# Kernel optimization log

Hardware: AMD Instinct MI355X
Metric: run time of the kernel (lower is better)

The kernel has to match this reference:

```python
import jax, jax.numpy as jnp
import numpy as np

N_LIG, N_TGT, E = 100000, 20000, 250000
LIG_IN, TGT_IN, H = 4, 1280, 128


def setup_inputs() -> dict:
    key = jax.random.key(0)
    ks = jax.random.split(key, 12)
    def lin_w(k, fan_in, fan_out):
        # kaiming-uniform-ish init, stored as [in, out] for x @ W
        bound = 1.0 / np.sqrt(fan_in)
        return jax.random.uniform(k, (fan_in, fan_out), jnp.float32, -bound, bound)
    return {
        "x_ligand": jax.random.normal(ks[0], (N_LIG, LIG_IN), jnp.float32),
        "x_target": jax.random.normal(ks[1], (N_TGT, TGT_IN), jnp.float32),
        "edge_src": jax.random.randint(ks[2], (E,), 0, N_LIG, jnp.int32),
        "edge_dst": jax.random.randint(ks[3], (E,), 0, N_TGT, jnp.int32),
        # SAGEConv (ligand -> target): lin_l on aggregated ligand msgs, lin_r on target self
        "W_lt_l": lin_w(ks[4], LIG_IN, H),
        "b_lt_l": jnp.zeros((H,), jnp.float32),
        "W_lt_r": lin_w(ks[5], TGT_IN, H),
        # SAGEConv (target -> ligand): lin_l on aggregated target msgs, lin_r on ligand self
        "W_tl_l": lin_w(ks[6], TGT_IN, H),
        "b_tl_l": jnp.zeros((H,), jnp.float32),
        "W_tl_r": lin_w(ks[7], LIG_IN, H),
        # edge predictor: Linear(2H -> 1)
        "W_ep": lin_w(ks[8], 2 * H, 1),
        "b_ep": jnp.zeros((1,), jnp.float32),
    }


def _mean_agg(x_src, src_idx, dst_idx, num_dst):
    # gather per-edge source features, scatter-mean onto destination nodes
    msg = x_src[src_idx]                                             # [E, F]
    s = jax.ops.segment_sum(msg, dst_idx, num_segments=num_dst)      # [N_dst, F]
    cnt = jax.ops.segment_sum(jnp.ones((src_idx.shape[0], 1), x_src.dtype),
                              dst_idx, num_segments=num_dst)         # [N_dst, 1]
    return s / jnp.maximum(cnt, 1.0)


def reference(x_ligand, x_target, edge_src, edge_dst,
              W_lt_l, b_lt_l, W_lt_r, W_tl_l, b_tl_l, W_tl_r, W_ep, b_ep):
    # SAGEConv (ligand, binds_to, target): aggregate ligand msgs into targets
    agg_t = _mean_agg(x_ligand, edge_src, edge_dst, N_TGT)           # [N_TGT, LIG_IN]
    t_out = agg_t @ W_lt_l + b_lt_l + x_target @ W_lt_r              # [N_TGT, H]
    # SAGEConv (target, binds_to, ligand): reversed edges (flip(0))
    agg_l = _mean_agg(x_target, edge_dst, edge_src, N_LIG)           # [N_LIG, TGT_IN]
    l_out = agg_l @ W_tl_l + b_tl_l + x_ligand @ W_tl_r              # [N_LIG, H]
    l_out = jax.nn.relu(l_out)
    t_out = jax.nn.relu(t_out)
    # edge predictor: gather endpoints, concat, linear, squeeze
    edge_feats = jnp.concatenate([l_out[edge_src], t_out[edge_dst]], axis=-1)  # [E, 2H]
    out = (edge_feats @ W_ep + b_ep).squeeze(-1)                     # [E]
    return out
```

## Files before the change

### kernel.cpp

```cpp
#include <hip/hip_runtime.h>
#include <hip/hip_bf16.h>


#define H 128
#define K_DIM 1280
#define LIG_IN 4
#define CAP_L 24
#define CAP_T 48

typedef __attribute__((ext_vector_type(8))) short bf16x8;
typedef __attribute__((ext_vector_type(4))) float f32x4;

#define AS1(p) ((const __attribute__((address_space(1))) void*)(p))
#define AS3(p) ((__attribute__((address_space(3))) void*)(p))

__global__ void fill_both(const int* __restrict__ src, const int* __restrict__ dst,
                          int* __restrict__ cur_l, int* __restrict__ cur_t,
                          int* __restrict__ adjd, int* __restrict__ adjs, int E)
{
    int e = blockIdx.x * blockDim.x + threadIdx.x;
    if (e >= E) return;
    int s = src[e], d = dst[e];
    int p = atomicAdd(&cur_l[s], 1);
    adjd[s * CAP_L + p] = d;
    int q = atomicAdd(&cur_t[d], 1);
    adjs[d * CAP_T + q] = s;
}

__global__ void cast_wt(const float* __restrict__ Wl, const float* __restrict__ Wr,
                        __hip_bfloat16* __restrict__ Wt, int n)
{
    int idx = blockIdx.x * blockDim.x + threadIdx.x;
    if (idx >= n) return;
    int nr = idx / K_DIM, k = idx - nr * K_DIM;
    float v = (nr < H) ? Wl[k * H + nr] : Wr[k * H + (nr - H)];
    Wt[idx] = __float2bfloat16(v);
}

__global__ __launch_bounds__(256)
void gemm_fused(const float* __restrict__ Xf,
                const unsigned short* __restrict__ Wt,
                float* __restrict__ y_tl, float* __restrict__ t_lin, int M)
{
    __shared__ short As[64 * 32];
    __shared__ short Bs[256 * 32];

    const int bm = blockIdx.x * 64;
    const int w = threadIdx.x >> 6, lane = threadIdx.x & 63;
    const int mrow = lane & 15, quad = lane >> 4;

    const int a_row = threadIdx.x >> 2;
    const int a_seg = threadIdx.x & 3;
    const float* gA = Xf + (size_t)min(bm + a_row, M - 1) * K_DIM + a_seg * 8;
    char* lA = (char*)As + a_row * 64 + a_seg * 16;

    const unsigned short* gB[4];
    char* lB[4];
#pragma unroll
    for (int i = 0; i < 4; ++i) {
        int q = i * 64 + lane;
        int row = w * 64 + (q >> 2);
        int seg = q & 3;
        gB[i] = Wt + (size_t)row * K_DIM + seg * 8;
        lB[i] = (char*)Bs + w * 4096 + i * 1024 + lane * 16;
    }

    f32x4 acc[4][4];
#pragma unroll
    for (int i = 0; i < 4; ++i)
#pragma unroll
        for (int j = 0; j < 4; ++j)
            acc[i][j] = (f32x4){0.f, 0.f, 0.f, 0.f};

    for (int k0 = 0; k0 < K_DIM; k0 += 32) {
#pragma unroll
        for (int i = 0; i < 4; ++i)
            __builtin_amdgcn_global_load_lds(AS1(gB[i] + k0), AS3(lB[i]), 16, 0, 0);
        float4 v0 = *(const float4*)(gA + k0);
        float4 v1 = *(const float4*)(gA + k0 + 4);
        union { __hip_bfloat16 h[8]; uint4 u; } r;
        r.h[0] = __float2bfloat16(v0.x); r.h[1] = __float2bfloat16(v0.y);
        r.h[2] = __float2bfloat16(v0.z); r.h[3] = __float2bfloat16(v0.w);
        r.h[4] = __float2bfloat16(v1.x); r.h[5] = __float2bfloat16(v1.y);
        r.h[6] = __float2bfloat16(v1.z); r.h[7] = __float2bfloat16(v1.w);
        *(uint4*)lA = r.u;
        __syncthreads();

        bf16x8 aF[4], bF[4];
#pragma unroll
        for (int i = 0; i < 4; ++i)
            aF[i] = *(const bf16x8*)((const char*)As + (i * 16 + mrow) * 64 + quad * 16);
#pragma unroll
        for (int j = 0; j < 4; ++j)
            bF[j] = *(const bf16x8*)((const char*)Bs + (w * 64 + j * 16 + mrow) * 64 + quad * 16);
#pragma unroll
        for (int i = 0; i < 4; ++i)
#pragma unroll
            for (int j = 0; j < 4; ++j)
                acc[i][j] = __builtin_amdgcn_mfma_f32_16x16x32_bf16(aF[i], bF[j], acc[i][j], 0, 0, 0);
        __syncthreads();
    }

    float* __restrict__ Y = (w < 2) ? y_tl : t_lin;
    const int cbase = (w & 1) * 64;
#pragma unroll
    for (int i = 0; i < 4; ++i) {
#pragma unroll
        for (int r = 0; r < 4; ++r) {
            int row = bm + i * 16 + quad * 4 + r;
            if (row < M) {
#pragma unroll
                for (int j = 0; j < 4; ++j) {
                    int col = cbase + j * 16 + mrow;
                    Y[(size_t)row * H + col] = acc[i][j][r];
                }
            }
        }
    }
}

__global__ void target_post(const int* __restrict__ cur_t, const int* __restrict__ adjs,
                            const float* __restrict__ xl, const float* __restrict__ t_lin,
                            const float* __restrict__ W_lt_l, const float* __restrict__ b_lt_l,
                            const float* __restrict__ W_ep,
                            float* __restrict__ st, int NT)
{
    int wid = (blockIdx.x * blockDim.x + threadIdx.x) >> 6;
    int lane = threadIdx.x & 63;
    if (wid >= NT) return;
    int cnt = cur_t[wid];
    float a0 = 0.f, a1 = 0.f, a2 = 0.f, a3 = 0.f;
    for (int j = lane; j < cnt; j += 64) {
        int s = adjs[wid * CAP_T + j];
        float4 v = *(const float4*)(xl + (size_t)s * LIG_IN);
        a0 += v.x; a1 += v.y; a2 += v.z; a3 += v.w;
    }
#pragma unroll
    for (int off = 32; off > 0; off >>= 1) {
        a0 += __shfl_xor(a0, off);
        a1 += __shfl_xor(a1, off);
        a2 += __shfl_xor(a2, off);
        a3 += __shfl_xor(a3, off);
    }
    float inv = 1.0f / fmaxf((float)cnt, 1.0f);
    a0 *= inv; a1 *= inv; a2 *= inv; a3 *= inv;
    float acc = 0.f;
#pragma unroll
    for (int p = 0; p < 2; ++p) {
        int h = lane + p * 64;
        float v = a0 * W_lt_l[h] + a1 * W_lt_l[H + h] + a2 * W_lt_l[2 * H + h] +
                  a3 * W_lt_l[3 * H + h] + b_lt_l[h] + t_lin[(size_t)wid * H + h];
        v = fmaxf(v, 0.f);
        acc += v * W_ep[H + h];
    }
#pragma unroll
    for (int off = 32; off > 0; off >>= 1) acc += __shfl_down(acc, off);
    if (lane == 0) st[wid] = acc;
}

__global__ void ligand_gather_post(const int* __restrict__ cur_l, const int* __restrict__ adjd,
                                   const float* __restrict__ y_tl,
                                   const float* __restrict__ xl,
                                   const float* __restrict__ W_tl_r, const float* __restrict__ b_tl_l,
                                   const float* __restrict__ W_ep,
                                   float* __restrict__ sl, int NL)
{
    int wid = (blockIdx.x * blockDim.x + threadIdx.x) >> 6;
    int lane = threadIdx.x & 63;
    if (wid >= NL) return;
    int cnt = cur_l[wid];
    float a0 = 0.f, a1 = 0.f;
    for (int j = 0; j < cnt; ++j) {
        int d = adjd[wid * CAP_L + j];
        const float* row = y_tl + (size_t)d * H;
        a0 += row[lane];
        a1 += row[lane + 64];
    }
    float inv = 1.0f / fmaxf((float)cnt, 1.0f);
    float4 x = *(const float4*)(xl + (size_t)wid * LIG_IN);
    float acc = 0.f;
    {
        int h = lane;
        float v = a0 * inv + b_tl_l[h] +
                  x.x * W_tl_r[h] + x.y * W_tl_r[H + h] +
                  x.z * W_tl_r[2 * H + h] + x.w * W_tl_r[3 * H + h];
        v = fmaxf(v, 0.f);
        acc += v * W_ep[h];
    }
    {
        int h = lane + 64;
        float v = a1 * inv + b_tl_l[h] +
                  x.x * W_tl_r[h] + x.y * W_tl_r[H + h] +
                  x.z * W_tl_r[2 * H + h] + x.w * W_tl_r[3 * H + h];
        v = fmaxf(v, 0.f);
        acc += v * W_ep[h];
    }
#pragma unroll
    for (int off = 32; off > 0; off >>= 1) acc += __shfl_down(acc, off);
    if (lane == 0) sl[wid] = acc;
}

__global__ void edge_out(const int* __restrict__ src, const int* __restrict__ dst,
                         const float* __restrict__ sl, const float* __restrict__ st,
                         const float* __restrict__ b_ep, float* __restrict__ out, int E)
{
    int e = blockIdx.x * blockDim.x + threadIdx.x;
    if (e >= E) return;
    out[e] = sl[src[e]] + st[dst[e]] + b_ep[0];
}

extern "C" void kernel_launch(void* const* d_in, const int* in_sizes, int n_in,
                              void* d_out, int out_size, void* d_ws, size_t ws_size,
                              hipStream_t stream) {
    const float* x_ligand = (const float*)d_in[0];
    const float* x_target = (const float*)d_in[1];
    const int*   edge_src = (const int*)d_in[2];
    const int*   edge_dst = (const int*)d_in[3];
    const float* W_lt_l   = (const float*)d_in[4];
    const float* b_lt_l   = (const float*)d_in[5];
    const float* W_lt_r   = (const float*)d_in[6];
    const float* W_tl_l   = (const float*)d_in[7];
    const float* b_tl_l   = (const float*)d_in[8];
    const float* W_tl_r   = (const float*)d_in[9];
    const float* W_ep     = (const float*)d_in[10];
    const float* b_ep     = (const float*)d_in[11];
    float* out = (float*)d_out;

    const int NL = in_sizes[0] / LIG_IN;
    const int NT = in_sizes[1] / K_DIM;
    const int E  = in_sizes[2];

    char* ws = (char*)d_ws;
    size_t off = 0;
    auto take = [&](size_t bytes) { size_t o = off; off += (bytes + 15) & ~(size_t)15; return o; };
    size_t off_Wt     = take((size_t)2 * H * K_DIM * 2);
    size_t off_y_tl   = take((size_t)NT * H * 4);
    size_t off_t_lin  = take((size_t)NT * H * 4);
    size_t off_adjd   = take((size_t)NL * CAP_L * 4);
    size_t off_adjs   = take((size_t)NT * CAP_T * 4);
    size_t off_cur_l  = take((size_t)NL * 4);
    size_t off_cur_t  = take((size_t)NT * 4);
    size_t off_sl     = take((size_t)NL * 4);
    size_t off_st     = take((size_t)NT * 4);
    if (off > ws_size) {
        hipMemsetAsync(d_out, 0, (size_t)out_size * 4, stream);
        return;
    }

    __hip_bfloat16* Wt = (__hip_bfloat16*)(ws + off_Wt);
    float* y_tl  = (float*)(ws + off_y_tl);
    float* t_lin = (float*)(ws + off_t_lin);
    int*   adjd  = (int*)(ws + off_adjd);
    int*   adjs  = (int*)(ws + off_adjs);
    int*   cur_l = (int*)(ws + off_cur_l);
    int*   cur_t = (int*)(ws + off_cur_t);
    float* sl    = (float*)(ws + off_sl);
    float* st    = (float*)(ws + off_st);

    hipMemsetAsync(cur_l, 0, off_sl - off_cur_l, stream);

    fill_both<<<(E + 255) / 256, 256, 0, stream>>>(edge_src, edge_dst,
                                                   cur_l, cur_t, adjd, adjs, E);
    int nw = 2 * H * K_DIM;
    cast_wt<<<(nw + 255) / 256, 256, 0, stream>>>(W_tl_l, W_lt_r, Wt, nw);

    int nMB = (NT + 63) / 64;
    gemm_fused<<<nMB, 256, 0, stream>>>(x_target, (const unsigned short*)Wt, y_tl, t_lin, NT);

    target_post<<<(NT * 64 + 255) / 256, 256, 0, stream>>>(cur_t, adjs, x_ligand, t_lin,
                                                           W_lt_l, b_lt_l, W_ep, st, NT);
    ligand_gather_post<<<(NL * 64 + 255) / 256, 256, 0, stream>>>(cur_l, adjd, y_tl, x_ligand,
                                                                  W_tl_r, b_tl_l, W_ep, sl, NL);
    edge_out<<<(E + 255) / 256, 256, 0, stream>>>(edge_src, edge_dst, sl, st, b_ep, out, E);
}
```

Baseline: 310.7 us.

## Double-buffer GEMM LDS tiles with 32-row blocks; vectorize ligand gather loads

The GEMM now uses 32-row M tiles, which doubles the block count to fill more CUs. It double-buffers the A and B LDS tiles so the next K-slice's global loads overlap the current MFMA work, with one barrier per iteration. The ligand gather reads each y_tl row as float2 per lane instead of two strided scalars, and the fill kernel is reordered after the GEMM launch. Dropping the row bound check assumes NT is a multiple of 32, and the smaller tile re-reads the weight matrix more often.

```diff
diff --git a/kernel.cpp b/kernel.cpp
--- a/kernel.cpp
+++ b/kernel.cpp
@@ -42,78 +42,92 @@
                 const unsigned short* __restrict__ Wt,
                 float* __restrict__ y_tl, float* __restrict__ t_lin, int M)
 {
-    __shared__ short As[64 * 32];
-    __shared__ short Bs[256 * 32];
-
-    const int bm = blockIdx.x * 64;
-    const int w = threadIdx.x >> 6, lane = threadIdx.x & 63;
+    __shared__ short As[2][32 * 32];
+    __shared__ short Bs[2][256 * 32];
+
+    const int bm = blockIdx.x * 32;
+    const int t = threadIdx.x;
+    const int w = t >> 6, lane = t & 63;
     const int mrow = lane & 15, quad = lane >> 4;
 
-    const int a_row = threadIdx.x >> 2;
-    const int a_seg = threadIdx.x & 3;
-    const float* gA = Xf + (size_t)min(bm + a_row, M - 1) * K_DIM + a_seg * 8;
-    char* lA = (char*)As + a_row * 64 + a_seg * 16;
+    const int a_row = t >> 3, a_seg = t & 7;
+    const float* gA = Xf + (size_t)(bm + a_row) * K_DIM + a_seg * 4;
+    const int lA_off = a_row * 64 + a_seg * 8;
 
     const unsigned short* gB[4];
-    char* lB[4];
-#pragma unroll
-    for (int i = 0; i < 4; ++i) {
-        int q = i * 64 + lane;
-        int row = w * 64 + (q >> 2);
-        int seg = q & 3;
-        gB[i] = Wt + (size_t)row * K_DIM + seg * 8;
-        lB[i] = (char*)Bs + w * 4096 + i * 1024 + lane * 16;
-    }
-
-    f32x4 acc[4][4];
-#pragma unroll
-    for (int i = 0; i < 4; ++i)
+    int lB_off[4];
+#pragma unroll
+    for (int r = 0; r < 4; ++r) {
+        int row = w * 64 + r * 16 + (lane >> 2);
+        int seg = lane & 3;
+        gB[r] = Wt + (size_t)row * K_DIM + seg * 8;
+        lB_off[r] = w * 4096 + r * 1024 + lane * 16;
+    }
+
+    f32x4 acc[2][4];
+#pragma unroll
+    for (int i = 0; i < 2; ++i)
 #pragma unroll
         for (int j = 0; j < 4; ++j)
             acc[i][j] = (f32x4){0.f, 0.f, 0.f, 0.f};
 
-    for (int k0 = 0; k0 < K_DIM; k0 += 32) {
-#pragma unroll
-        for (int i = 0; i < 4; ++i)
-            __builtin_amdgcn_global_load_lds(AS1(gB[i] + k0), AS3(lB[i]), 16, 0, 0);
-        float4 v0 = *(const float4*)(gA + k0);
-        float4 v1 = *(const float4*)(gA + k0 + 4);
-        union { __hip_bfloat16 h[8]; uint4 u; } r;
-        r.h[0] = __float2bfloat16(v0.x); r.h[1] = __float2bfloat16(v0.y);
-        r.h[2] = __float2bfloat16(v0.z); r.h[3] = __float2bfloat16(v0.w);
-        r.h[4] = __float2bfloat16(v1.x); r.h[5] = __float2bfloat16(v1.y);
-        r.h[6] = __float2bfloat16(v1.z); r.h[7] = __float2bfloat16(v1.w);
-        *(uint4*)lA = r.u;
-        __syncthreads();
-
-        bf16x8 aF[4], bF[4];
-#pragma unroll
-        for (int i = 0; i < 4; ++i)
-            aF[i] = *(const bf16x8*)((const char*)As + (i * 16 + mrow) * 64 + quad * 16);
+#pragma unroll
+    for (int r = 0; r < 4; ++r)
+        __builtin_amdgcn_global_load_lds(AS1(gB[r]), AS3((char*)Bs[0] + lB_off[r]), 16, 0, 0);
+    {
+        float4 v = *(const float4*)gA;
+        union { __hip_bfloat16 h[4]; uint2 u; } c;
+        c.h[0] = __float2bfloat16(v.x); c.h[1] = __float2bfloat16(v.y);
+        c.h[2] = __float2bfloat16(v.z); c.h[3] = __float2bfloat16(v.w);
+        *(uint2*)((char*)As[0] + lA_off) = c.u;
+    }
+    __syncthreads();
+
+    const int NK = K_DIM / 32;
+    for (int k = 0; k < NK; ++k) {
+        const int cur = k & 1, nxt = cur ^ 1;
+        float4 vn;
+        if (k + 1 < NK) {
+#pragma unroll
+            for (int r = 0; r < 4; ++r)
+                __builtin_amdgcn_global_load_lds(AS1(gB[r] + (k + 1) * 32),
+                                                 AS3((char*)Bs[nxt] + lB_off[r]), 16, 0, 0);
+            vn = *(const float4*)(gA + (k + 1) * 32);
+        }
+
+        bf16x8 aF[2], bF[4];
+#pragma unroll
+        for (int i = 0; i < 2; ++i)
+            aF[i] = *(const bf16x8*)((const char*)As[cur] + (i * 16 + mrow) * 64 + quad * 16);
 #pragma unroll
         for (int j = 0; j < 4; ++j)
-            bF[j] = *(const bf16x8*)((const char*)Bs + (w * 64 + j * 16 + mrow) * 64 + quad * 16);
-#pragma unroll
-        for (int i = 0; i < 4; ++i)
+            bF[j] = *(const bf16x8*)((const char*)Bs[cur] + (w * 64 + j * 16 + mrow) * 64 + quad * 16);
+#pragma unroll
+        for (int i = 0; i < 2; ++i)
 #pragma unroll
             for (int j = 0; j < 4; ++j)
                 acc[i][j] = __builtin_amdgcn_mfma_f32_16x16x32_bf16(aF[i], bF[j], acc[i][j], 0, 0, 0);
+
+        if (k + 1 < NK) {
+            union { __hip_bfloat16 h[4]; uint2 u; } c;
+            c.h[0] = __float2bfloat16(vn.x); c.h[1] = __float2bfloat16(vn.y);
+            c.h[2] = __float2bfloat16(vn.z); c.h[3] = __float2bfloat16(vn.w);
+            *(uint2*)((char*)As[nxt] + lA_off) = c.u;
+        }
         __syncthreads();
     }
 
     float* __restrict__ Y = (w < 2) ? y_tl : t_lin;
     const int cbase = (w & 1) * 64;
 #pragma unroll
-    for (int i = 0; i < 4; ++i) {
+    for (int i = 0; i < 2; ++i) {
 #pragma unroll
         for (int r = 0; r < 4; ++r) {
             int row = bm + i * 16 + quad * 4 + r;
-            if (row < M) {
-#pragma unroll
-                for (int j = 0; j < 4; ++j) {
-                    int col = cbase + j * 16 + mrow;
-                    Y[(size_t)row * H + col] = acc[i][j][r];
-                }
+#pragma unroll
+            for (int j = 0; j < 4; ++j) {
+                int col = cbase + j * 16 + mrow;
+                Y[(size_t)row * H + col] = acc[i][j][r];
             }
         }
     }
@@ -172,15 +186,15 @@
     float a0 = 0.f, a1 = 0.f;
     for (int j = 0; j < cnt; ++j) {
         int d = adjd[wid * CAP_L + j];
-        const float* row = y_tl + (size_t)d * H;
-        a0 += row[lane];
-        a1 += row[lane + 64];
+        float2 f = ((const float2*)(y_tl + (size_t)d * H))[lane];
+        a0 += f.x;
+        a1 += f.y;
     }
     float inv = 1.0f / fmaxf((float)cnt, 1.0f);
     float4 x = *(const float4*)(xl + (size_t)wid * LIG_IN);
     float acc = 0.f;
     {
-        int h = lane;
+        int h = 2 * lane;
         float v = a0 * inv + b_tl_l[h] +
                   x.x * W_tl_r[h] + x.y * W_tl_r[H + h] +
                   x.z * W_tl_r[2 * H + h] + x.w * W_tl_r[3 * H + h];
@@ -188,7 +202,7 @@
         acc += v * W_ep[h];
     }
     {
-        int h = lane + 64;
+        int h = 2 * lane + 1;
         float v = a1 * inv + b_tl_l[h] +
                   x.x * W_tl_r[h] + x.y * W_tl_r[H + h] +
                   x.z * W_tl_r[2 * H + h] + x.w * W_tl_r[3 * H + h];
@@ -259,13 +273,13 @@
 
     hipMemsetAsync(cur_l, 0, off_sl - off_cur_l, stream);
 
+    int nw = 2 * H * K_DIM;
+    cast_wt<<<(nw + 255) / 256, 256, 0, stream>>>(W_tl_l, W_lt_r, Wt, nw);
+
+    gemm_fused<<<NT / 32, 256, 0, stream>>>(x_target, (const unsigned short*)Wt, y_tl, t_lin, NT);
+
     fill_both<<<(E + 255) / 256, 256, 0, stream>>>(edge_src, edge_dst,
                                                    cur_l, cur_t, adjd, adjs, E);
-    int nw = 2 * H * K_DIM;
-    cast_wt<<<(nw + 255) / 256, 256, 0, stream>>>(W_tl_l, W_lt_r, Wt, nw);
-
-    int nMB = (NT + 63) / 64;
-    gemm_fused<<<nMB, 256, 0, stream>>>(x_target, (const unsigned short*)Wt, y_tl, t_lin, NT);
 
     target_post<<<(NT * 64 + 255) / 256, 256, 0, stream>>>(cur_t, adjs, x_ligand, t_lin,
                                                            W_lt_l, b_lt_l, W_ep, st, NT);
```

Result: slower. 319.6 us (+2.9%).
